# Kernel optimization log

Measured on AMD Instinct MI355X. Metric: run time of the kernel, lower is better.

Reference implementation:

```python
import jax, jax.numpy as jnp
import numpy as np
from jax import lax

H1, H2, H3, T, IN = 15, 60, 20, 15, 1


def lstm_layer(x, W_ih, W_hh, b_ih, b_hh):
    # x: [B, T, in] -> hs: [B, T, H]; PyTorch gate order i, f, g, o
    B = x.shape[0]
    H = W_hh.shape[1]
    h0 = jnp.zeros((B, H), x.dtype)
    c0 = jnp.zeros((B, H), x.dtype)
    b = b_ih + b_hh

    def step(carry, xt):
        h, c = carry
        g = xt @ W_ih.T + h @ W_hh.T + b  # [B, 4H]
        i, f, gg, o = jnp.split(g, 4, axis=-1)
        i = jax.nn.sigmoid(i)
        f = jax.nn.sigmoid(f)
        gg = jnp.tanh(gg)
        o = jax.nn.sigmoid(o)
        c = f * c + i * gg
        h = o * jnp.tanh(c)
        return (h, c), h

    _, hs = lax.scan(step, (h0, c0), jnp.swapaxes(x, 0, 1))  # hs: [T, B, H]
    return jnp.swapaxes(hs, 0, 1)


def setup_inputs() -> dict:
    key = jax.random.key(0)
    ks = jax.random.split(key, 16)
    s = 0.1
    B = 131072
    inp = {
        "x": jax.random.normal(ks[0], (B, T, IN), jnp.float32),
        "W_ih0": jax.random.normal(ks[1], (4 * H1, IN), jnp.float32) * s,
        "W_hh0": jax.random.normal(ks[2], (4 * H1, H1), jnp.float32) * s,
        "b_ih0": jax.random.normal(ks[3], (4 * H1,), jnp.float32) * s,
        "b_hh0": jax.random.normal(ks[4], (4 * H1,), jnp.float32) * s,
        "W_ih1": jax.random.normal(ks[5], (4 * H1, H1), jnp.float32) * s,
        "W_hh1": jax.random.normal(ks[6], (4 * H1, H1), jnp.float32) * s,
        "b_ih1": jax.random.normal(ks[7], (4 * H1,), jnp.float32) * s,
        "b_hh1": jax.random.normal(ks[8], (4 * H1,), jnp.float32) * s,
        "W1": jax.random.normal(ks[9], (H2, H1), jnp.float32) * s,
        "b1": jax.random.normal(ks[10], (H2,), jnp.float32) * s,
        "W2": jax.random.normal(ks[11], (H3, H2), jnp.float32) * s,
        "b2": jax.random.normal(ks[12], (H3,), jnp.float32) * s,
        "W3": jax.random.normal(ks[13], (1, H3), jnp.float32) * s,
        "b3": jax.random.normal(ks[14], (1,), jnp.float32) * s,
    }
    return inp


def reference(x, W_ih0, W_hh0, b_ih0, b_hh0, W_ih1, W_hh1, b_ih1, b_hh1, W1, b1, W2, b2, W3, b3):
    h1 = lstm_layer(x, W_ih0, W_hh0, b_ih0, b_hh0)   # [B, T, H1]
    h2 = lstm_layer(h1, W_ih1, W_hh1, b_ih1, b_hh1)  # [B, T, H1] (eval mode: no dropout)
    feat = h2[:, :, -1]                              # [B, T] == [B, 15]
    out1 = feat @ W1.T + b1                          # [B, 60]
    out2 = out1 @ W2.T + b2                          # [B, 20]
    out = out2 @ W3.T + b3                           # [B, 1]
    return out
```

## Files before the change

### kernel.cpp

```cpp
#include <hip/hip_runtime.h>

#define HH   15
#define TT   15
#define NH2  60
#define NH3  20

#define LOG2E 1.44269504088896340736f
#define L2E2  2.88539008177792680736f

typedef _Float16 f16x8 __attribute__((ext_vector_type(8)));
typedef float    f32x4 __attribute__((ext_vector_type(4)));

#define WS_V  2048
#define WS_CB 2063

__device__ __forceinline__ float fast_rcp(float x)  { return __builtin_amdgcn_rcpf(x); }
__device__ __forceinline__ float fast_exp2(float x) { return __builtin_amdgcn_exp2f(x); }

__global__ void lstm_prep(const float* __restrict__ Wih0, const float* __restrict__ Whh0,
                          const float* __restrict__ bih0, const float* __restrict__ bhh0,
                          const float* __restrict__ Wih1, const float* __restrict__ Whh1,
                          const float* __restrict__ bih1, const float* __restrict__ bhh1,
                          const float* __restrict__ W1, const float* __restrict__ b1,
                          const float* __restrict__ W2, const float* __restrict__ b2,
                          const float* __restrict__ W3, const float* __restrict__ b3,
                          float* __restrict__ wsf)
{
    const int tid = threadIdx.x;
    unsigned* wsu = (unsigned*)wsf;

    {
        const int f = tid >> 6, l = tid & 63;
        const int n = f & 3;
        const bool isL2 = (f >= 4);
        const int u = l & 15, g = l >> 4;
        const float sc = (n == 2) ? L2E2 : LOG2E;
        const int r = n * 15 + (u < 15 ? u : 0);
        float vals[8];
        #pragma unroll
        for (int j = 0; j < 8; ++j) {
            const int k = g * 8 + j;
            float v = 0.0f;
            if (u < 15) {
                if (!isL2) {
                    if (k < 15)       v = Whh0[r * 15 + k];
                    else if (k == 15) v = Wih0[r];
                    else if (k == 16) v = bih0[r] + bhh0[r];
                } else {
                    if (k < 15)       v = Wih1[r * 15 + k];
                    else if (k == 15) v = bih1[r] + bhh1[r];
                    else if (k < 31)  v = Whh1[r * 15 + (k - 16)];
                }
            }
            vals[j] = v * sc;
        }
        #pragma unroll
        for (int d = 0; d < 4; ++d) {
            union { _Float16 h[2]; unsigned u32; } p;
            p.h[0] = (_Float16)vals[2 * d];
            p.h[1] = (_Float16)vals[2 * d + 1];
            wsu[f * 256 + l * 4 + d] = p.u32;
        }
    }

    __shared__ float sU[NH2];
    if (tid < NH2) {
        float ua = 0.0f;
        #pragma unroll
        for (int k = 0; k < NH3; ++k) ua = fmaf(W3[k], W2[k * NH2 + tid], ua);
        sU[tid] = ua;
    }
    __syncthreads();
    if (tid < TT) {
        float v = 0.0f;
        for (int j = 0; j < NH2; ++j) v = fmaf(sU[j], W1[j * HH + tid], v);
        wsf[WS_V + tid] = v;
    }
    if (tid == 0) {
        float c = b3[0];
        for (int k = 0; k < NH3; ++k) c = fmaf(W3[k], b2[k], c);
        for (int j = 0; j < NH2; ++j) c = fmaf(sU[j], b1[j], c);
        wsf[WS_CB] = c;
    }
}

__global__ __launch_bounds__(256)
void lstm_mfma(const float* __restrict__ x, const float* __restrict__ wsf,
               float* __restrict__ out, int B)
{
    __shared__ __align__(16) _Float16 lds[4][2][16][40];

    const int tid = threadIdx.x;
    const int wid = tid >> 6;
    const int l   = tid & 63;
    const int u   = l & 15;
    const int g   = l >> 4;
    const int wbase = (blockIdx.x * 4 + wid) * 16;

    {
        unsigned* zw = (unsigned*)&lds[wid][0][0][0];
        #pragma unroll
        for (int i = 0; i < 10; ++i) zw[l + 64 * i] = 0u;
    }

    const uint4* wsq = (const uint4*)wsf;
    union FU { uint4 q; f16x8 h; };
#define LOADB(name, fidx) f16x8 name; { FU t_; t_.q = wsq[(fidx) * 64 + l]; name = t_.h; }
    LOADB(B0, 0) LOADB(B1, 1) LOADB(B2, 2) LOADB(B3, 3)
    LOADB(B4, 4) LOADB(B5, 5) LOADB(B6, 6) LOADB(B7, 7)
#undef LOADB

    if (l < 16) {
        lds[wid][0][l][16] = (_Float16)1.0f;
        lds[wid][1][l][15] = (_Float16)1.0f;
    }

    const int u1col = (u == 15) ? 31 : u;

    const float cb = wsf[WS_CB];
    f32x4 acc = {cb, cb, cb, cb};
    f32x4 c1  = {0.0f, 0.0f, 0.0f, 0.0f};
    f32x4 c2  = {0.0f, 0.0f, 0.0f, 0.0f};
    const f32x4 zc = {0.0f, 0.0f, 0.0f, 0.0f};

    const float* xrow = x + (size_t)(wbase + u) * TT;

#define MFMA(a, b, c) __builtin_amdgcn_mfma_f32_16x16x32_f16((a), (b), (c), 0, 0, 0)

#define UPD1(i) { \
        const float ei = fast_exp2(-d0[i]); \
        const float ef = fast_exp2(-d1[i]); \
        const float eg = fast_exp2(d2[i]); \
        const float eo = fast_exp2(-d3[i]); \
        const float itg = (eg - 1.0f) * fast_rcp((1.0f + ei) * (eg + 1.0f)); \
        const float cc = fmaf(fast_rcp(1.0f + ef), c1[i], itg); \
        c1[i] = cc; \
        const float ec = fast_exp2(L2E2 * cc); \
        const float hh = (ec - 1.0f) * fast_rcp((1.0f + eo) * (ec + 1.0f)); \
        const _Float16 hf = (_Float16)hh; \
        lds[wid][0][4 * g + (i)][u] = hf; \
        lds[wid][1][4 * g + (i)][u1col] = hf; }

#define UPD2(i) { \
        const float ei = fast_exp2(-e0[i]); \
        const float ef = fast_exp2(-e1[i]); \
        const float eg = fast_exp2(e2[i]); \
        const float eo = fast_exp2(-e3[i]); \
        const float itg = (eg - 1.0f) * fast_rcp((1.0f + ei) * (eg + 1.0f)); \
        const float cc = fmaf(fast_rcp(1.0f + ef), c2[i], itg); \
        c2[i] = cc; \
        const float ec = fast_exp2(L2E2 * cc); \
        const float hh = (ec - 1.0f) * fast_rcp((1.0f + eo) * (ec + 1.0f)); \
        lds[wid][1][4 * g + (i)][16 + u] = (_Float16)hh; \
        acc[i] = fmaf(hh, vt, acc[i]); }

    if (l < 16) lds[wid][0][l][15] = (_Float16)xrow[0];
    f16x8 a1 = *(const f16x8*)&lds[wid][0][u][g * 8];
    f32x4 d0 = MFMA(a1, B0, zc);
    f32x4 d1 = MFMA(a1, B1, zc);
    f32x4 d2 = MFMA(a1, B2, zc);
    f32x4 d3 = MFMA(a1, B3, zc);

    #pragma unroll 2
    for (int t = 0; t < TT - 1; ++t) {
        UPD1(0) UPD1(1) UPD1(2) UPD1(3)

        const f16x8 a2 = *(const f16x8*)&lds[wid][1][u][g * 8];
        f32x4 e0 = MFMA(a2, B4, zc);
        f32x4 e1 = MFMA(a2, B5, zc);
        f32x4 e2 = MFMA(a2, B6, zc);
        f32x4 e3 = MFMA(a2, B7, zc);

        if (l < 16) lds[wid][0][l][15] = (_Float16)xrow[t + 1];
        a1 = *(const f16x8*)&lds[wid][0][u][g * 8];
        d0 = MFMA(a1, B0, zc);
        d1 = MFMA(a1, B1, zc);
        d2 = MFMA(a1, B2, zc);
        d3 = MFMA(a1, B3, zc);

        const float vt = wsf[WS_V + t];
        UPD2(0) UPD2(1) UPD2(2) UPD2(3)
    }

    {
        UPD1(0) UPD1(1) UPD1(2) UPD1(3)
        const f16x8 a2 = *(const f16x8*)&lds[wid][1][u][g * 8];
        f32x4 e0 = MFMA(a2, B4, zc);
        f32x4 e1 = MFMA(a2, B5, zc);
        f32x4 e2 = MFMA(a2, B6, zc);
        f32x4 e3 = MFMA(a2, B7, zc);
        const float vt = wsf[WS_V + (TT - 1)];
        UPD2(0) UPD2(1) UPD2(2) UPD2(3)
    }
#undef UPD1
#undef UPD2
#undef MFMA

    if (u == 14) {
        out[wbase + 4 * g + 0] = acc[0];
        out[wbase + 4 * g + 1] = acc[1];
        out[wbase + 4 * g + 2] = acc[2];
        out[wbase + 4 * g + 3] = acc[3];
    }
}

extern "C" void kernel_launch(void* const* d_in, const int* in_sizes, int n_in,
                              void* d_out, int out_size, void* d_ws, size_t ws_size,
                              hipStream_t stream) {
    (void)n_in; (void)ws_size; (void)out_size;
    const float* x    = (const float*)d_in[0];
    const float* Wih0 = (const float*)d_in[1];
    const float* Whh0 = (const float*)d_in[2];
    const float* bih0 = (const float*)d_in[3];
    const float* bhh0 = (const float*)d_in[4];
    const float* Wih1 = (const float*)d_in[5];
    const float* Whh1 = (const float*)d_in[6];
    const float* bih1 = (const float*)d_in[7];
    const float* bhh1 = (const float*)d_in[8];
    const float* W1   = (const float*)d_in[9];
    const float* b1   = (const float*)d_in[10];
    const float* W2   = (const float*)d_in[11];
    const float* b2   = (const float*)d_in[12];
    const float* W3   = (const float*)d_in[13];
    const float* b3   = (const float*)d_in[14];
    float* out = (float*)d_out;
    float* wsf = (float*)d_ws;

    const int B = in_sizes[0] / TT;

    lstm_prep<<<1, 512, 0, stream>>>(Wih0, Whh0, bih0, bhh0,
                                     Wih1, Whh1, bih1, bhh1,
                                     W1, b1, W2, b2, W3, b3, wsf);

    const int grid = B / (16 * 4);
    lstm_mfma<<<grid, 256, 0, stream>>>(x, wsf, out, B);
}
```

Before: 145.7 us.

## Process two 16-row batch tiles per wave to interleave independent LSTM chains

Each wave now handles 32 batch rows as two independent 16-row tiles, interleaving their MFMA and gate-update sequences so one tile's transcendental work can hide the other's MFMA and LDS latency. The grid is halved to match. The cell-state update is also rewritten to use a single reciprocal instead of two, and the x load for the next step is issued earlier in the loop. In exchange, register pressure per thread roughly doubles and fewer waves are launched, which may reduce occupancy and latency hiding across waves.

```diff
diff --git a/kernel.cpp b/kernel.cpp
--- a/kernel.cpp
+++ b/kernel.cpp
@@ -88,19 +88,19 @@
 void lstm_mfma(const float* __restrict__ x, const float* __restrict__ wsf,
                float* __restrict__ out, int B)
 {
-    __shared__ __align__(16) _Float16 lds[4][2][16][40];
+    __shared__ __align__(16) _Float16 lds[4][2][2][16][40];
 
     const int tid = threadIdx.x;
     const int wid = tid >> 6;
     const int l   = tid & 63;
     const int u   = l & 15;
     const int g   = l >> 4;
-    const int wbase = (blockIdx.x * 4 + wid) * 16;
-
-    {
-        unsigned* zw = (unsigned*)&lds[wid][0][0][0];
-        #pragma unroll
-        for (int i = 0; i < 10; ++i) zw[l + 64 * i] = 0u;
+    const int wbase = (blockIdx.x * 4 + wid) * 32;
+
+    {
+        unsigned* zw = (unsigned*)&lds[wid][0][0][0][0];
+        #pragma unroll
+        for (int i = 0; i < 20; ++i) zw[l + 64 * i] = 0u;
     }
 
     const uint4* wsq = (const uint4*)wsf;
@@ -111,96 +111,124 @@
 #undef LOADB
 
     if (l < 16) {
-        lds[wid][0][l][16] = (_Float16)1.0f;
-        lds[wid][1][l][15] = (_Float16)1.0f;
+        lds[wid][0][0][l][16] = (_Float16)1.0f;
+        lds[wid][0][1][l][15] = (_Float16)1.0f;
+        lds[wid][1][0][l][16] = (_Float16)1.0f;
+        lds[wid][1][1][l][15] = (_Float16)1.0f;
     }
 
     const int u1col = (u == 15) ? 31 : u;
 
     const float cb = wsf[WS_CB];
-    f32x4 acc = {cb, cb, cb, cb};
-    f32x4 c1  = {0.0f, 0.0f, 0.0f, 0.0f};
-    f32x4 c2  = {0.0f, 0.0f, 0.0f, 0.0f};
-    const f32x4 zc = {0.0f, 0.0f, 0.0f, 0.0f};
-
-    const float* xrow = x + (size_t)(wbase + u) * TT;
+    f32x4 accA = {cb, cb, cb, cb}, accB = accA;
+    f32x4 c1A = {0.f,0.f,0.f,0.f}, c2A = c1A, c1B = c1A, c2B = c1A;
+    const f32x4 zc = {0.f,0.f,0.f,0.f};
+
+    const int til = (l >> 4) & 1;
+    const float* xp = x + (size_t)(wbase + (l & 31)) * TT;
 
 #define MFMA(a, b, c) __builtin_amdgcn_mfma_f32_16x16x32_f16((a), (b), (c), 0, 0, 0)
 
-#define UPD1(i) { \
+#define UPDC(i, d0, d1, d2, d3, Cst) \
         const float ei = fast_exp2(-d0[i]); \
         const float ef = fast_exp2(-d1[i]); \
         const float eg = fast_exp2(d2[i]); \
         const float eo = fast_exp2(-d3[i]); \
-        const float itg = (eg - 1.0f) * fast_rcp((1.0f + ei) * (eg + 1.0f)); \
-        const float cc = fmaf(fast_rcp(1.0f + ef), c1[i], itg); \
-        c1[i] = cc; \
-        const float ec = fast_exp2(L2E2 * cc); \
-        const float hh = (ec - 1.0f) * fast_rcp((1.0f + eo) * (ec + 1.0f)); \
+        const float dn1 = (1.0f + ei) * (eg + 1.0f); \
+        const float dn2 = 1.0f + ef; \
+        const float t1 = fmaf(L2E2, eg, -L2E2); \
+        const float r  = fast_rcp(dn1 * dn2); \
+        const float cc = fmaf(Cst[i], dn1, t1 * dn2) * r; \
+        Cst[i] = cc; \
+        const float ec = fast_exp2(cc); \
+        const float hh = (ec - 1.0f) * fast_rcp((1.0f + eo) * (ec + 1.0f));
+
+#define UPD1(i, T, Cst, d0, d1, d2, d3) { \
+        UPDC(i, d0, d1, d2, d3, Cst) \
         const _Float16 hf = (_Float16)hh; \
-        lds[wid][0][4 * g + (i)][u] = hf; \
-        lds[wid][1][4 * g + (i)][u1col] = hf; }
-
-#define UPD2(i) { \
-        const float ei = fast_exp2(-e0[i]); \
-        const float ef = fast_exp2(-e1[i]); \
-        const float eg = fast_exp2(e2[i]); \
-        const float eo = fast_exp2(-e3[i]); \
-        const float itg = (eg - 1.0f) * fast_rcp((1.0f + ei) * (eg + 1.0f)); \
-        const float cc = fmaf(fast_rcp(1.0f + ef), c2[i], itg); \
-        c2[i] = cc; \
-        const float ec = fast_exp2(L2E2 * cc); \
-        const float hh = (ec - 1.0f) * fast_rcp((1.0f + eo) * (ec + 1.0f)); \
-        lds[wid][1][4 * g + (i)][16 + u] = (_Float16)hh; \
-        acc[i] = fmaf(hh, vt, acc[i]); }
-
-    if (l < 16) lds[wid][0][l][15] = (_Float16)xrow[0];
-    f16x8 a1 = *(const f16x8*)&lds[wid][0][u][g * 8];
-    f32x4 d0 = MFMA(a1, B0, zc);
-    f32x4 d1 = MFMA(a1, B1, zc);
-    f32x4 d2 = MFMA(a1, B2, zc);
-    f32x4 d3 = MFMA(a1, B3, zc);
+        lds[wid][T][0][4 * g + (i)][u] = hf; \
+        lds[wid][T][1][4 * g + (i)][u1col] = hf; }
+
+#define UPD2(i, T, Cst, Acc, e0, e1, e2, e3) { \
+        UPDC(i, e0, e1, e2, e3, Cst) \
+        lds[wid][T][1][4 * g + (i)][16 + u] = (_Float16)hh; \
+        Acc[i] = fmaf(hh, vt, Acc[i]); }
+
+    {
+        const float x0 = xp[0];
+        if (l < 32) lds[wid][til][0][u][15] = (_Float16)x0;
+    }
+    f16x8 a1A = *(const f16x8*)&lds[wid][0][0][u][g * 8];
+    f16x8 a1B = *(const f16x8*)&lds[wid][1][0][u][g * 8];
+    f32x4 dA0 = MFMA(a1A, B0, zc), dA1 = MFMA(a1A, B1, zc);
+    f32x4 dA2 = MFMA(a1A, B2, zc), dA3 = MFMA(a1A, B3, zc);
+    f32x4 dB0 = MFMA(a1B, B0, zc), dB1 = MFMA(a1B, B1, zc);
+    f32x4 dB2 = MFMA(a1B, B2, zc), dB3 = MFMA(a1B, B3, zc);
 
     #pragma unroll 2
     for (int t = 0; t < TT - 1; ++t) {
-        UPD1(0) UPD1(1) UPD1(2) UPD1(3)
-
-        const f16x8 a2 = *(const f16x8*)&lds[wid][1][u][g * 8];
-        f32x4 e0 = MFMA(a2, B4, zc);
-        f32x4 e1 = MFMA(a2, B5, zc);
-        f32x4 e2 = MFMA(a2, B6, zc);
-        f32x4 e3 = MFMA(a2, B7, zc);
-
-        if (l < 16) lds[wid][0][l][15] = (_Float16)xrow[t + 1];
-        a1 = *(const f16x8*)&lds[wid][0][u][g * 8];
-        d0 = MFMA(a1, B0, zc);
-        d1 = MFMA(a1, B1, zc);
-        d2 = MFMA(a1, B2, zc);
-        d3 = MFMA(a1, B3, zc);
+        const float xn = xp[t + 1];
+
+        UPD1(0, 0, c1A, dA0, dA1, dA2, dA3) UPD1(1, 0, c1A, dA0, dA1, dA2, dA3)
+        UPD1(2, 0, c1A, dA0, dA1, dA2, dA3) UPD1(3, 0, c1A, dA0, dA1, dA2, dA3)
+        UPD1(0, 1, c1B, dB0, dB1, dB2, dB3) UPD1(1, 1, c1B, dB0, dB1, dB2, dB3)
+        UPD1(2, 1, c1B, dB0, dB1, dB2, dB3) UPD1(3, 1, c1B, dB0, dB1, dB2, dB3)
+
+        const f16x8 a2A = *(const f16x8*)&lds[wid][0][1][u][g * 8];
+        f32x4 eA0 = MFMA(a2A, B4, zc), eA1 = MFMA(a2A, B5, zc);
+        f32x4 eA2 = MFMA(a2A, B6, zc), eA3 = MFMA(a2A, B7, zc);
+        const f16x8 a2B = *(const f16x8*)&lds[wid][1][1][u][g * 8];
+        f32x4 eB0 = MFMA(a2B, B4, zc), eB1 = MFMA(a2B, B5, zc);
+        f32x4 eB2 = MFMA(a2B, B6, zc), eB3 = MFMA(a2B, B7, zc);
+
+        if (l < 32) lds[wid][til][0][u][15] = (_Float16)xn;
+        a1A = *(const f16x8*)&lds[wid][0][0][u][g * 8];
+        dA0 = MFMA(a1A, B0, zc); dA1 = MFMA(a1A, B1, zc);
+        dA2 = MFMA(a1A, B2, zc); dA3 = MFMA(a1A, B3, zc);
+        a1B = *(const f16x8*)&lds[wid][1][0][u][g * 8];
+        dB0 = MFMA(a1B, B0, zc); dB1 = MFMA(a1B, B1, zc);
+        dB2 = MFMA(a1B, B2, zc); dB3 = MFMA(a1B, B3, zc);
 
         const float vt = wsf[WS_V + t];
-        UPD2(0) UPD2(1) UPD2(2) UPD2(3)
-    }
-
-    {
-        UPD1(0) UPD1(1) UPD1(2) UPD1(3)
-        const f16x8 a2 = *(const f16x8*)&lds[wid][1][u][g * 8];
-        f32x4 e0 = MFMA(a2, B4, zc);
-        f32x4 e1 = MFMA(a2, B5, zc);
-        f32x4 e2 = MFMA(a2, B6, zc);
-        f32x4 e3 = MFMA(a2, B7, zc);
+        UPD2(0, 0, c2A, accA, eA0, eA1, eA2, eA3) UPD2(1, 0, c2A, accA, eA0, eA1, eA2, eA3)
+        UPD2(2, 0, c2A, accA, eA0, eA1, eA2, eA3) UPD2(3, 0, c2A, accA, eA0, eA1, eA2, eA3)
+        UPD2(0, 1, c2B, accB, eB0, eB1, eB2, eB3) UPD2(1, 1, c2B, accB, eB0, eB1, eB2, eB3)
+        UPD2(2, 1, c2B, accB, eB0, eB1, eB2, eB3) UPD2(3, 1, c2B, accB, eB0, eB1, eB2, eB3)
+    }
+
+    {
+        UPD1(0, 0, c1A, dA0, dA1, dA2, dA3) UPD1(1, 0, c1A, dA0, dA1, dA2, dA3)
+        UPD1(2, 0, c1A, dA0, dA1, dA2, dA3) UPD1(3, 0, c1A, dA0, dA1, dA2, dA3)
+        UPD1(0, 1, c1B, dB0, dB1, dB2, dB3) UPD1(1, 1, c1B, dB0, dB1, dB2, dB3)
+        UPD1(2, 1, c1B, dB0, dB1, dB2, dB3) UPD1(3, 1, c1B, dB0, dB1, dB2, dB3)
+
+        const f16x8 a2A = *(const f16x8*)&lds[wid][0][1][u][g * 8];
+        f32x4 eA0 = MFMA(a2A, B4, zc), eA1 = MFMA(a2A, B5, zc);
+        f32x4 eA2 = MFMA(a2A, B6, zc), eA3 = MFMA(a2A, B7, zc);
+        const f16x8 a2B = *(const f16x8*)&lds[wid][1][1][u][g * 8];
+        f32x4 eB0 = MFMA(a2B, B4, zc), eB1 = MFMA(a2B, B5, zc);
+        f32x4 eB2 = MFMA(a2B, B6, zc), eB3 = MFMA(a2B, B7, zc);
+
         const float vt = wsf[WS_V + (TT - 1)];
-        UPD2(0) UPD2(1) UPD2(2) UPD2(3)
+        UPD2(0, 0, c2A, accA, eA0, eA1, eA2, eA3) UPD2(1, 0, c2A, accA, eA0, eA1, eA2, eA3)
+        UPD2(2, 0, c2A, accA, eA0, eA1, eA2, eA3) UPD2(3, 0, c2A, accA, eA0, eA1, eA2, eA3)
+        UPD2(0, 1, c2B, accB, eB0, eB1, eB2, eB3) UPD2(1, 1, c2B, accB, eB0, eB1, eB2, eB3)
+        UPD2(2, 1, c2B, accB, eB0, eB1, eB2, eB3) UPD2(3, 1, c2B, accB, eB0, eB1, eB2, eB3)
     }
 #undef UPD1
 #undef UPD2
+#undef UPDC
 #undef MFMA
 
     if (u == 14) {
-        out[wbase + 4 * g + 0] = acc[0];
-        out[wbase + 4 * g + 1] = acc[1];
-        out[wbase + 4 * g + 2] = acc[2];
-        out[wbase + 4 * g + 3] = acc[3];
+        out[wbase + 4 * g + 0] = accA[0];
+        out[wbase + 4 * g + 1] = accA[1];
+        out[wbase + 4 * g + 2] = accA[2];
+        out[wbase + 4 * g + 3] = accA[3];
+        out[wbase + 16 + 4 * g + 0] = accB[0];
+        out[wbase + 16 + 4 * g + 1] = accB[1];
+        out[wbase + 16 + 4 * g + 2] = accB[2];
+        out[wbase + 16 + 4 * g + 3] = accB[3];
     }
 }
 
@@ -232,6 +260,6 @@
                                      Wih1, Whh1, bih1, bhh1,
                                      W1, b1, W2, b2, W3, b3, wsf);
 
-    const int grid = B / (16 * 4);
+    const int grid = B / (32 * 4);
     lstm_mfma<<<grid, 256, 0, stream>>>(x, wsf, out, B);
 }
```

Result: no change. 143.1 us (-1.8%).
